# Optimization experiments

Hardware: AMD Instinct MI355X
Metric: run time of the kernel (lower is better)

The kernel has to match this reference:

```python
import jax, jax.numpy as jnp
import numpy as np

N, M, E, DIM = 100000, 2000, 400000, 128
GIN = 2 * DIM + 3  # gate MLP input width


def _mlp2(x, W1, b1, W2, b2):
    # Linear -> ReLU -> Linear
    return jnp.maximum(x @ W1 + b1, 0.0) @ W2 + b2


def setup_inputs() -> dict:
    key = jax.random.key(0)
    ks = jax.random.split(key, 20)
    s = lambda fan_in: 1.0 / np.sqrt(fan_in)
    inp = {
        "res_feat": jax.random.normal(ks[0], (N, DIM), jnp.float32),
        "meta_feat": jax.random.normal(ks[1], (M, DIM), jnp.float32),
        "sec_ids": jax.random.randint(ks[2], (N,), 0, M),
        "batch_pe_vector": jax.random.normal(ks[3], (N, 3), jnp.float32),
        "batch_meta_2_node_edge": jax.random.randint(ks[4], (2, E), 0, M),
        "batch_meta_2_node_vector": jax.random.normal(ks[5], (E, 3), jnp.float32),
        # gate1 params
        "g1_W1": jax.random.uniform(ks[6], (GIN, DIM), jnp.float32, -s(GIN), s(GIN)),
        "g1_b1": jnp.zeros((DIM,), jnp.float32),
        "g1_W2": jax.random.uniform(ks[7], (DIM, DIM), jnp.float32, -s(DIM), s(DIM)),
        "g1_b2": jnp.zeros((DIM,), jnp.float32),
        # gate2 params
        "g2_W1": jax.random.uniform(ks[8], (GIN, DIM), jnp.float32, -s(GIN), s(GIN)),
        "g2_b1": jnp.zeros((DIM,), jnp.float32),
        "g2_W2": jax.random.uniform(ks[9], (DIM, DIM), jnp.float32, -s(DIM), s(DIM)),
        "g2_b2": jnp.zeros((DIM,), jnp.float32),
        # fuse params
        "f_W1": jax.random.uniform(ks[10], (DIM, DIM), jnp.float32, -s(DIM), s(DIM)),
        "f_b1": jnp.zeros((DIM,), jnp.float32),
        "f_W2": jax.random.uniform(ks[11], (DIM, DIM), jnp.float32, -s(DIM), s(DIM)),
        "f_b2": jnp.zeros((DIM,), jnp.float32),
    }
    return inp


def reference(res_feat, meta_feat, sec_ids, batch_pe_vector,
              batch_meta_2_node_edge, batch_meta_2_node_vector,
              g1_W1, g1_b1, g1_W2, g1_b2,
              g2_W1, g2_b1, g2_W2, g2_b2,
              f_W1, f_b1, f_W2, f_b2):
    n = res_feat.shape[0]
    # gate1: per-node gather of meta features
    meta_broadcast = meta_feat[sec_ids]                       # [N, dim]
    gate1_in = jnp.concatenate([res_feat, meta_broadcast, -batch_pe_vector], axis=-1)
    gate1_w = _mlp2(gate1_in, g1_W1, g1_b1, g1_W2, g1_b2)     # [N, dim]
    # gate2: per-edge gathers
    src, dst = batch_meta_2_node_edge[0], batch_meta_2_node_edge[1]
    meta_add = meta_feat[src]                                 # [E, dim]
    res_b = res_feat[dst]                                     # [E, dim]
    gate2_in = jnp.concatenate([res_b, meta_add, batch_meta_2_node_vector], axis=-1)
    gate2_w = _mlp2(gate2_in, g2_W1, g2_b1, g2_W2, g2_b2)     # [E, dim]
    # scatter_mean over destination nodes
    vals = gate2_w * meta_add
    sums = jax.ops.segment_sum(vals, dst, num_segments=n)
    cnts = jax.ops.segment_sum(jnp.ones((vals.shape[0],), vals.dtype), dst, num_segments=n)
    meta_add_fea = sums / jnp.maximum(cnts, 1.0)[:, None]
    fused = res_feat + gate1_w * meta_broadcast + meta_add_fea
    return _mlp2(fused, f_W1, f_b1, f_W2, f_b2)
```

## Files before the change

### kernel.cpp

```cpp
#include <hip/hip_runtime.h>


typedef short bf16x8 __attribute__((ext_vector_type(8)));
typedef float f32x4  __attribute__((ext_vector_type(4)));

#define XS_PAD 136
#define F_PAD  132

__device__ __forceinline__ unsigned short f2bf(float f){
  union { float f; unsigned u; } v; v.f = f;
  return (unsigned short)((v.u + 0x7FFFu + ((v.u >> 16) & 1u)) >> 16);
}
__device__ __forceinline__ unsigned pack2(float a, float b){
  return (unsigned)f2bf(a) | ((unsigned)f2bf(b) << 16);
}
__device__ __forceinline__ float bf2f(unsigned short u){
  union { unsigned u; float f; } v; v.u = ((unsigned)u) << 16; return v.f;
}

__device__ __forceinline__ void mfma_layer(const unsigned short* Xs,
                                           const bf16x8 (&B)[2][4],
                                           int lane, f32x4 (&acc)[4][2]) {
  const int lcol = lane & 15, quad = lane >> 4;
  #pragma unroll
  for (int rg = 0; rg < 4; ++rg) {
    bf16x8 A[4];
    const unsigned short* ab = Xs + (rg*16 + lcol)*XS_PAD + quad*8;
    #pragma unroll
    for (int kk = 0; kk < 4; ++kk) A[kk] = *(const bf16x8*)(ab + kk*32);
    #pragma unroll
    for (int ctl = 0; ctl < 2; ++ctl)
      #pragma unroll
      for (int kk = 0; kk < 4; ++kk)
        acc[rg][ctl] = __builtin_amdgcn_mfma_f32_16x16x32_bf16(
            A[kk], B[ctl][kk], acc[rg][ctl], 0, 0, 0);
  }
}

__device__ __forceinline__ void load_bfrags(const unsigned short* __restrict__ Wt,
                                            int wave, int lane, bf16x8 (&B)[2][4]) {
  const int lcol = lane & 15, quad = lane >> 4;
  #pragma unroll
  for (int ctl = 0; ctl < 2; ++ctl) {
    int col = (wave*2 + ctl)*16 + lcol;
    #pragma unroll
    for (int kk = 0; kk < 4; ++kk)
      B[ctl][kk] = *(const bf16x8*)(Wt + (size_t)col*128 + kk*32 + quad*8);
  }
}

__device__ __forceinline__ void zero_acc(f32x4 (&acc)[4][2]) {
  #pragma unroll
  for (int rg = 0; rg < 4; ++rg)
    #pragma unroll
    for (int ctl = 0; ctl < 2; ++ctl) {
      acc[rg][ctl][0]=0.f; acc[rg][ctl][1]=0.f;
      acc[rg][ctl][2]=0.f; acc[rg][ctl][3]=0.f;
    }
}

struct WPtrs { const float* s[8]; };
__global__ __launch_bounds__(256) void transpose_w8(WPtrs p,
                                                    unsigned short* __restrict__ dstbase) {
  int slab = blockIdx.x >> 4, blk = blockIdx.x & 15;
  const float* W = p.s[slab];
  unsigned short* Wt = dstbase + (size_t)slab*16384;
  int c  = blk*8 + (threadIdx.x >> 5);
  int k0 = (threadIdx.x & 31) * 4;
  unsigned short o[4];
  #pragma unroll
  for (int j = 0; j < 4; ++j) o[j] = f2bf(W[(size_t)(k0 + j)*128 + c]);
  *(uint2*)(Wt + (size_t)c*128 + k0) =
      make_uint2((unsigned)o[0] | ((unsigned)o[1] << 16),
                 (unsigned)o[2] | ((unsigned)o[3] << 16));
}

__global__ __launch_bounds__(256) void a2_mfma(const float* __restrict__ res,
                                               const unsigned short* __restrict__ WAt,
                                               float* __restrict__ A2, int mrows) {
  __shared__ __align__(16) unsigned short Xs[64*XS_PAD];
  const int t = threadIdx.x, lane = t & 63, wave = t >> 6;
  const int quad = lane >> 4, lcol = lane & 15;
  const int tile0 = blockIdx.x * 64;
  bf16x8 B[2][4];
  load_bfrags(WAt, wave, lane, B);
  #pragma unroll
  for (int i = 0; i < 8; ++i) {
    int f = t + i*256, row = f >> 5, c4 = f & 31;
    int gr = tile0 + row;
    float4 v = make_float4(0.f,0.f,0.f,0.f);
    if (gr < mrows) v = *(const float4*)(res + (size_t)gr*128 + c4*4);
    *(uint2*)(Xs + row*XS_PAD + c4*4) = make_uint2(pack2(v.x,v.y), pack2(v.z,v.w));
  }
  __syncthreads();
  f32x4 acc[4][2]; zero_acc(acc);
  mfma_layer(Xs, B, lane, acc);
  #pragma unroll
  for (int rg = 0; rg < 4; ++rg)
    #pragma unroll
    for (int ctl = 0; ctl < 2; ++ctl) {
      int col = (wave*2 + ctl)*16 + lcol;
      #pragma unroll
      for (int reg = 0; reg < 4; ++reg) {
        int gr = tile0 + rg*16 + quad*4 + reg;
        if (gr < mrows) A2[(size_t)gr*128 + col] = acc[rg][ctl][reg];
      }
    }
}

__global__ void hist_kernel(const int* __restrict__ dst, int* __restrict__ counts, int E){
  int e = blockIdx.x*256 + threadIdx.x;
  if (e < E) atomicAdd(&counts[dst[e]], 1);
}
__global__ void scan1(const int* __restrict__ counts, int* __restrict__ exoff,
                      int* __restrict__ blocksum, int N){
  __shared__ int s[256];
  int t = threadIdx.x, gid = blockIdx.x*256 + t;
  int v = (gid < N) ? counts[gid] : 0;
  s[t] = v; __syncthreads();
  for (int off = 1; off < 256; off <<= 1){
    int x = (t >= off) ? s[t-off] : 0; __syncthreads();
    s[t] += x; __syncthreads();
  }
  if (gid < N) exoff[gid] = s[t] - v;
  if (t == 255) blocksum[blockIdx.x] = s[255];
}
__global__ void scan2(int* __restrict__ blocksum, int nb){
  __shared__ int s[512];
  int t = threadIdx.x;
  int v = (t < nb) ? blocksum[t] : 0;
  s[t] = v; __syncthreads();
  for (int off = 1; off < 512; off <<= 1){
    int x = (t >= off) ? s[t-off] : 0; __syncthreads();
    s[t] += x; __syncthreads();
  }
  if (t < nb) blocksum[t] = s[t] - v;
}
__global__ void scan3(int* __restrict__ exoff, const int* __restrict__ blockbase,
                      int* __restrict__ cursor, int N){
  int gid = blockIdx.x*256 + threadIdx.x;
  if (gid < N){ int v = exoff[gid] + blockbase[gid >> 8]; exoff[gid] = v; cursor[gid] = v; }
}
__global__ void fill_kernel(const int* __restrict__ dst, int* __restrict__ cursor,
                            int* __restrict__ edge_ids, int E){
  int e = blockIdx.x*256 + threadIdx.x;
  if (e < E){ int p = atomicAdd(&cursor[dst[e]], 1); edge_ids[p] = e; }
}

__global__ __launch_bounds__(256) void edge_mfma(
    const float* __restrict__ A2, const float* __restrict__ meta,
    const float* __restrict__ evec, const int* __restrict__ src,
    const int* __restrict__ edge_ids, const int* __restrict__ row_start,
    const int* __restrict__ counts,
    const float* __restrict__ g2W1full, const float* __restrict__ b1,
    const unsigned short* __restrict__ g2Bt, const unsigned short* __restrict__ W2t,
    const float* __restrict__ b2, float* __restrict__ SUM) {
  const int n = blockIdx.x;
  const int count = counts[n];
  if (count == 0) return;
  __shared__ __align__(16) unsigned short Xm[64*XS_PAD];
  __shared__ __align__(16) unsigned short Xh[64*XS_PAD];
  __shared__ __align__(16) float base[128];
  __shared__ __align__(16) float Wc[3*128];
  __shared__ float b2s[128];
  __shared__ int srcl[64];
  __shared__ float evl[64*3];
  const int t = threadIdx.x, lane = t & 63, wave = t >> 6;
  const int quad = lane >> 4, lcol = lane & 15;
  const int rs = row_start[n];

  bf16x8 BB[2][4], BW2[2][4];
  load_bfrags(g2Bt, wave, lane, BB);
  load_bfrags(W2t,  wave, lane, BW2);
  if (t < 128) {
    base[t]   = A2[(size_t)n*128 + t] + b1[t];
    b2s[t]    = b2[t];
    Wc[t]     = g2W1full[256*128 + t];
    Wc[128+t] = g2W1full[257*128 + t];
    Wc[256+t] = g2W1full[258*128 + t];
  }
  float sv0 = 0.f, sv1 = 0.f;

  for (int t0 = 0; t0 < count; t0 += 64) {
    __syncthreads();
    if (t < 64) {
      int idx = t0 + t;
      int s = 0; float e0=0.f,e1=0.f,e2=0.f;
      if (idx < count) {
        int e = edge_ids[rs + idx];
        s = src[e];
        e0 = evec[(size_t)e*3]; e1 = evec[(size_t)e*3+1]; e2 = evec[(size_t)e*3+2];
      }
      srcl[t] = s; evl[t*3] = e0; evl[t*3+1] = e1; evl[t*3+2] = e2;
    }
    __syncthreads();
    #pragma unroll
    for (int i = 0; i < 8; ++i) {
      int f = t + i*256, row = f >> 5, c4 = f & 31;
      float4 v = make_float4(0.f,0.f,0.f,0.f);
      if (t0 + row < count)
        v = *(const float4*)(meta + (size_t)srcl[row]*128 + c4*4);
      *(uint2*)(Xm + row*XS_PAD + c4*4) = make_uint2(pack2(v.x,v.y), pack2(v.z,v.w));
    }
    __syncthreads();
    f32x4 acc[4][2]; zero_acc(acc);
    mfma_layer(Xm, BB, lane, acc);
    #pragma unroll
    for (int rg = 0; rg < 4; ++rg)
      #pragma unroll
      for (int ctl = 0; ctl < 2; ++ctl) {
        int col = (wave*2 + ctl)*16 + lcol;
        #pragma unroll
        for (int reg = 0; reg < 4; ++reg) {
          int row = rg*16 + quad*4 + reg;
          float hv = acc[rg][ctl][reg] + base[col]
                   + evl[row*3]*Wc[col] + evl[row*3+1]*Wc[128+col]
                   + evl[row*3+2]*Wc[256+col];
          Xh[row*XS_PAD + col] = f2bf(fmaxf(hv, 0.f));
        }
      }
    __syncthreads();
    zero_acc(acc);
    mfma_layer(Xh, BW2, lane, acc);
    #pragma unroll
    for (int ctl = 0; ctl < 2; ++ctl) {
      int col = (wave*2 + ctl)*16 + lcol;
      float b2v = b2s[col];
      float s_acc = 0.f;
      #pragma unroll
      for (int rg = 0; rg < 4; ++rg)
        #pragma unroll
        for (int reg = 0; reg < 4; ++reg) {
          int rl = rg*16 + quad*4 + reg;
          if (t0 + rl < count)
            s_acc += (acc[rg][ctl][reg] + b2v) * bf2f(Xm[rl*XS_PAD + col]);
        }
      if (ctl == 0) sv0 += s_acc; else sv1 += s_acc;
    }
  }
  sv0 += __shfl_xor(sv0, 16, 64); sv0 += __shfl_xor(sv0, 32, 64);
  sv1 += __shfl_xor(sv1, 16, 64); sv1 += __shfl_xor(sv1, 32, 64);
  if (quad == 0) {
    SUM[(size_t)n*128 + (wave*2 + 0)*16 + lcol] = sv0;
    SUM[(size_t)n*128 + (wave*2 + 1)*16 + lcol] = sv1;
  }
}

__global__ __launch_bounds__(256) void fused_node(
    const float* __restrict__ res, const float* __restrict__ meta,
    const int* __restrict__ sec_ids, const float* __restrict__ pe,
    const float* __restrict__ g1W1full,
    const unsigned short* __restrict__ g1At, const unsigned short* __restrict__ g1Bt,
    const unsigned short* __restrict__ g1W2t, const float* __restrict__ g1b1,
    const float* __restrict__ g1b2,
    const unsigned short* __restrict__ fW1t, const float* __restrict__ fb1v,
    const unsigned short* __restrict__ fW2t, const float* __restrict__ fb2v,
    const float* __restrict__ SUM, const int* __restrict__ counts, int msize,
    float* __restrict__ out, int rows) {
  __shared__ __align__(16) unsigned short Xall[2*64*XS_PAD];
  unsigned short* Xa = Xall;
  unsigned short* Xm = Xall + 64*XS_PAD;
  float* F = (float*)Xall;
  __shared__ __align__(16) float Wc[3*128];
  __shared__ float b1s[128], b2s[128], fb1s[128], fb2s[128];
  __shared__ int   sids[64];
  __shared__ float pel[64*3];
  __shared__ float inv[64];
  const int t = threadIdx.x, lane = t & 63, wave = t >> 6;
  const int quad = lane >> 4, lcol = lane & 15;
  const int tile0 = blockIdx.x * 64;

  if (t < 128) {
    b1s[t] = g1b1[t]; b2s[t] = g1b2[t]; fb1s[t] = fb1v[t]; fb2s[t] = fb2v[t];
    Wc[t]     = g1W1full[256*128 + t];
    Wc[128+t] = g1W1full[257*128 + t];
    Wc[256+t] = g1W1full[258*128 + t];
  }
  if (t < 64) {
    int gr = tile0 + t;
    sids[t] = (gr < rows) ? sec_ids[gr] : 0;
    float p0=0.f,p1=0.f,p2=0.f;
    if (gr < rows){ p0=pe[(size_t)gr*3]; p1=pe[(size_t)gr*3+1]; p2=pe[(size_t)gr*3+2]; }
    pel[t*3]=p0; pel[t*3+1]=p1; pel[t*3+2]=p2;
    int c = (gr < rows && gr < msize) ? counts[gr] : 0;
    inv[t] = (c > 0) ? 1.f/(float)c : 0.f;
  }
  __syncthreads();

  bf16x8 BA[2][4], BB[2][4];
  load_bfrags(g1At, wave, lane, BA);
  load_bfrags(g1Bt, wave, lane, BB);

  #pragma unroll
  for (int i = 0; i < 8; ++i) {
    int f = t + i*256, row = f >> 5, c4 = f & 31;
    int gr = tile0 + row;
    float4 rv = make_float4(0.f,0.f,0.f,0.f);
    float4 mv = make_float4(0.f,0.f,0.f,0.f);
    if (gr < rows) {
      rv = *(const float4*)(res  + (size_t)gr*128 + c4*4);
      mv = *(const float4*)(meta + (size_t)sids[row]*128 + c4*4);
    }
    *(uint2*)(Xa + row*XS_PAD + c4*4) = make_uint2(pack2(rv.x,rv.y), pack2(rv.z,rv.w));
    *(uint2*)(Xm + row*XS_PAD + c4*4) = make_uint2(pack2(mv.x,mv.y), pack2(mv.z,mv.w));
  }
  __syncthreads();

  f32x4 acc[4][2]; zero_acc(acc);
  mfma_layer(Xa, BA, lane, acc);
  mfma_layer(Xm, BB, lane, acc);
  __syncthreads();
  #pragma unroll
  for (int rg = 0; rg < 4; ++rg)
    #pragma unroll
    for (int ctl = 0; ctl < 2; ++ctl) {
      int col = (wave*2 + ctl)*16 + lcol;
      #pragma unroll
      for (int reg = 0; reg < 4; ++reg) {
        int row = rg*16 + quad*4 + reg;
        float sm = b1s[col] - pel[row*3]*Wc[col]
                 - pel[row*3+1]*Wc[128+col] - pel[row*3+2]*Wc[256+col];
        Xa[row*XS_PAD + col] = f2bf(fmaxf(acc[rg][ctl][reg] + sm, 0.f));
      }
    }
  __syncthreads();
  bf16x8 B2g[2][4]; load_bfrags(g1W2t, wave, lane, B2g);
  zero_acc(acc);
  mfma_layer(Xa, B2g, lane, acc);
  __syncthreads();
  #pragma unroll
  for (int rg = 0; rg < 4; ++rg)
    #pragma unroll
    for (int ctl = 0; ctl < 2; ++ctl) {
      int col = (wave*2 + ctl)*16 + lcol;
      #pragma unroll
      for (int reg = 0; reg < 4; ++reg)
        Xa[(rg*16 + quad*4 + reg)*XS_PAD + col] = f2bf(acc[rg][ctl][reg] + b2s[col]);
    }
  __syncthreads();
  #pragma unroll
  for (int i = 0; i < 8; ++i) {
    int f = t + i*256, row = f >> 5, c4 = f & 31;
    int gr = tile0 + row;
    if (gr < rows) {
      float4 rv = *(const float4*)(res + (size_t)gr*128 + c4*4);
      uint2 gu = *(const uint2*)(Xa + row*XS_PAD + c4*4);
      uint2 mu = *(const uint2*)(Xm + row*XS_PAD + c4*4);
      float g0 = bf2f((unsigned short)(gu.x & 0xFFFF)), g1 = bf2f((unsigned short)(gu.x >> 16));
      float g2 = bf2f((unsigned short)(gu.y & 0xFFFF)), g3 = bf2f((unsigned short)(gu.y >> 16));
      float m0 = bf2f((unsigned short)(mu.x & 0xFFFF)), m1 = bf2f((unsigned short)(mu.x >> 16));
      float m2 = bf2f((unsigned short)(mu.y & 0xFFFF)), m3 = bf2f((unsigned short)(mu.y >> 16));
      float iv = inv[row];
      float s0=0.f,s1=0.f,s2=0.f,s3=0.f;
      if (iv > 0.f) {
        float4 s = *(const float4*)(SUM + (size_t)gr*128 + c4*4);
        s0 = s.x*iv; s1 = s.y*iv; s2 = s.z*iv; s3 = s.w*iv;
      }
      float f0 = rv.x + g0*m0 + s0, f1 = rv.y + g1*m1 + s1;
      float f2v = rv.z + g2*m2 + s2, f3 = rv.w + g3*m3 + s3;
      *(uint2*)(Xm + row*XS_PAD + c4*4) = make_uint2(pack2(f0,f1), pack2(f2v,f3));
    }
  }
  __syncthreads();
  bf16x8 BF1[2][4]; load_bfrags(fW1t, wave, lane, BF1);
  zero_acc(acc);
  mfma_layer(Xm, BF1, lane, acc);
  #pragma unroll
  for (int rg = 0; rg < 4; ++rg)
    #pragma unroll
    for (int ctl = 0; ctl < 2; ++ctl) {
      int col = (wave*2 + ctl)*16 + lcol;
      #pragma unroll
      for (int reg = 0; reg < 4; ++reg)
        Xa[(rg*16 + quad*4 + reg)*XS_PAD + col] =
            f2bf(fmaxf(acc[rg][ctl][reg] + fb1s[col], 0.f));
    }
  __syncthreads();
  bf16x8 BF2[2][4]; load_bfrags(fW2t, wave, lane, BF2);
  zero_acc(acc);
  mfma_layer(Xa, BF2, lane, acc);
  __syncthreads();
  #pragma unroll
  for (int rg = 0; rg < 4; ++rg)
    #pragma unroll
    for (int ctl = 0; ctl < 2; ++ctl) {
      int col = (wave*2 + ctl)*16 + lcol;
      #pragma unroll
      for (int reg = 0; reg < 4; ++reg)
        F[(rg*16 + quad*4 + reg)*F_PAD + col] = acc[rg][ctl][reg] + fb2s[col];
    }
  __syncthreads();
  #pragma unroll
  for (int i = 0; i < 8; ++i) {
    int f = t + i*256, row = f >> 5, c4 = f & 31;
    int gr = tile0 + row;
    if (gr < rows)
      *(float4*)(out + (size_t)gr*128 + c4*4) = *(const float4*)(F + row*F_PAD + c4*4);
  }
}

extern "C" void kernel_launch(void* const* d_in, const int* in_sizes, int n_in,
                              void* d_out, int out_size, void* d_ws, size_t ws_size,
                              hipStream_t stream) {
  const float* res     = (const float*)d_in[0];
  const float* meta    = (const float*)d_in[1];
  const int*   sec_ids = (const int*)  d_in[2];
  const float* pe      = (const float*)d_in[3];
  const int*   edge    = (const int*)  d_in[4];
  const float* evec    = (const float*)d_in[5];
  const float* g1W1 = (const float*)d_in[6];
  const float* g1b1 = (const float*)d_in[7];
  const float* g1W2 = (const float*)d_in[8];
  const float* g1b2 = (const float*)d_in[9];
  const float* g2W1 = (const float*)d_in[10];
  const float* g2b1 = (const float*)d_in[11];
  const float* g2W2 = (const float*)d_in[12];
  const float* g2b2 = (const float*)d_in[13];
  const float* fW1  = (const float*)d_in[14];
  const float* fb1  = (const float*)d_in[15];
  const float* fW2  = (const float*)d_in[16];
  const float* fb2  = (const float*)d_in[17];

  const int N = in_sizes[0] / 128;
  const int M = in_sizes[1] / 128;
  const int E = in_sizes[4] / 2;
  const int* src = edge;
  const int* dst = edge + E;

  float* ws = (float*)d_ws;
  float* A2   = ws;
  float* SUMb = A2 + (size_t)M*128;
  int* counts     = (int*)(SUMb + (size_t)M*128);
  int* row_startp = counts + M;
  int* cursor     = row_startp + M;
  int* blocksum   = cursor + M;
  int* edge_ids   = blocksum + 512;
  uintptr_t wp = (uintptr_t)(edge_ids + E);
  wp = (wp + 15) & ~(uintptr_t)15;
  unsigned short* Wt = (unsigned short*)wp;
  unsigned short* W_g1A  = Wt + 0*16384;
  unsigned short* W_g1B  = Wt + 1*16384;
  unsigned short* W_g1W2 = Wt + 2*16384;
  unsigned short* W_g2A  = Wt + 3*16384;
  unsigned short* W_g2B  = Wt + 4*16384;
  unsigned short* W_g2W2 = Wt + 5*16384;
  unsigned short* W_fW1  = Wt + 6*16384;
  unsigned short* W_fW2  = Wt + 7*16384;
  float* out = (float*)d_out;

  hipMemsetAsync(counts, 0, (size_t)M*sizeof(int), stream);
  hipMemsetAsync(SUMb, 0, (size_t)M*128*sizeof(float), stream);

  WPtrs p;
  p.s[0] = g1W1;            p.s[1] = g1W1 + 128*128;  p.s[2] = g1W2;
  p.s[3] = g2W1;            p.s[4] = g2W1 + 128*128;  p.s[5] = g2W2;
  p.s[6] = fW1;             p.s[7] = fW2;
  transpose_w8<<<128, 256, 0, stream>>>(p, Wt);

  const int nbMt = (M + 63) / 64;
  const int nbN  = (N + 63) / 64;
  const int nbE  = (E + 255) / 256;
  const int nbS  = (M + 255) / 256;

  a2_mfma<<<nbMt, 256, 0, stream>>>(res, W_g2A, A2, M);

  hist_kernel<<<nbE, 256, 0, stream>>>(dst, counts, E);
  scan1<<<nbS, 256, 0, stream>>>(counts, row_startp, blocksum, M);
  scan2<<<1, 512, 0, stream>>>(blocksum, nbS);
  scan3<<<nbS, 256, 0, stream>>>(row_startp, blocksum, cursor, M);
  fill_kernel<<<nbE, 256, 0, stream>>>(dst, cursor, edge_ids, E);

  edge_mfma<<<M, 256, 0, stream>>>(A2, meta, evec, src, edge_ids,
                                   row_startp, counts, g2W1, g2b1,
                                   W_g2B, W_g2W2, g2b2, SUMb);

  fused_node<<<nbN, 256, 0, stream>>>(res, meta, sec_ids, pe, g1W1,
                                      W_g1A, W_g1B, W_g1W2, g1b1, g1b2,
                                      W_fW1, fb1, W_fW2, fb2,
                                      SUMb, counts, M, out, N);
}
```

Before: 419.9 us.

## Precompute meta@W1B per meta row, split edge segments across blocks with atomics

New measurement: 400.6 us. 4.6% less time.

```diff
diff --git a/kernel.cpp b/kernel.cpp
--- a/kernel.cpp
+++ b/kernel.cpp
@@ -5,7 +5,7 @@
 typedef float f32x4  __attribute__((ext_vector_type(4)));
 
 #define XS_PAD 136
-#define F_PAD  132
+#define S_SPLIT 4
 
 __device__ __forceinline__ unsigned short f2bf(float f){
   union { float f; unsigned u; } v; v.f = f;
@@ -75,21 +75,27 @@
                  (unsigned)o[2] | ((unsigned)o[3] << 16));
 }
 
-__global__ __launch_bounds__(256) void a2_mfma(const float* __restrict__ res,
-                                               const unsigned short* __restrict__ WAt,
-                                               float* __restrict__ A2, int mrows) {
+__global__ __launch_bounds__(256) void prep_mfma(const float* __restrict__ res,
+                                                 const float* __restrict__ meta,
+                                                 const unsigned short* __restrict__ WAt,
+                                                 const unsigned short* __restrict__ WBt,
+                                                 float* __restrict__ A2,
+                                                 float* __restrict__ M2, int mrows) {
   __shared__ __align__(16) unsigned short Xs[64*XS_PAD];
   const int t = threadIdx.x, lane = t & 63, wave = t >> 6;
   const int quad = lane >> 4, lcol = lane & 15;
   const int tile0 = blockIdx.x * 64;
+  const float* X = blockIdx.y ? meta : res;
+  const unsigned short* Wt = blockIdx.y ? WBt : WAt;
+  float* Y = blockIdx.y ? M2 : A2;
   bf16x8 B[2][4];
-  load_bfrags(WAt, wave, lane, B);
+  load_bfrags(Wt, wave, lane, B);
   #pragma unroll
   for (int i = 0; i < 8; ++i) {
     int f = t + i*256, row = f >> 5, c4 = f & 31;
     int gr = tile0 + row;
     float4 v = make_float4(0.f,0.f,0.f,0.f);
-    if (gr < mrows) v = *(const float4*)(res + (size_t)gr*128 + c4*4);
+    if (gr < mrows) v = *(const float4*)(X + (size_t)gr*128 + c4*4);
     *(uint2*)(Xs + row*XS_PAD + c4*4) = make_uint2(pack2(v.x,v.y), pack2(v.z,v.w));
   }
   __syncthreads();
@@ -103,7 +109,7 @@
       #pragma unroll
       for (int reg = 0; reg < 4; ++reg) {
         int gr = tile0 + rg*16 + quad*4 + reg;
-        if (gr < mrows) A2[(size_t)gr*128 + col] = acc[rg][ctl][reg];
+        if (gr < mrows) Y[(size_t)gr*128 + col] = acc[rg][ctl][reg];
       }
     }
 }
@@ -148,45 +154,47 @@
 }
 
 __global__ __launch_bounds__(256) void edge_mfma(
-    const float* __restrict__ A2, const float* __restrict__ meta,
-    const float* __restrict__ evec, const int* __restrict__ src,
-    const int* __restrict__ edge_ids, const int* __restrict__ row_start,
-    const int* __restrict__ counts,
-    const float* __restrict__ g2W1full, const float* __restrict__ b1,
-    const unsigned short* __restrict__ g2Bt, const unsigned short* __restrict__ W2t,
-    const float* __restrict__ b2, float* __restrict__ SUM) {
-  const int n = blockIdx.x;
+    const float* __restrict__ A2, const float* __restrict__ M2,
+    const float* __restrict__ meta, const float* __restrict__ evec,
+    const int* __restrict__ src, const int* __restrict__ edge_ids,
+    const int* __restrict__ row_start, const int* __restrict__ counts,
+    const float* __restrict__ b1, const float* __restrict__ g2W1full,
+    const unsigned short* __restrict__ W2t, const float* __restrict__ b2,
+    float* __restrict__ SUM) {
+  const int n = blockIdx.x / S_SPLIT, k = blockIdx.x % S_SPLIT;
   const int count = counts[n];
-  if (count == 0) return;
-  __shared__ __align__(16) unsigned short Xm[64*XS_PAD];
+  const int per = (count + S_SPLIT - 1) / S_SPLIT;
+  const int lo = k * per;
+  int hi = lo + per; if (hi > count) hi = count;
+  const int cnt = hi - lo;
+  if (cnt <= 0) return;
+  const int rs = row_start[n] + lo;
+
   __shared__ __align__(16) unsigned short Xh[64*XS_PAD];
-  __shared__ __align__(16) float base[128];
-  __shared__ __align__(16) float Wc[3*128];
-  __shared__ float b2s[128];
   __shared__ int srcl[64];
   __shared__ float evl[64*3];
   const int t = threadIdx.x, lane = t & 63, wave = t >> 6;
   const int quad = lane >> 4, lcol = lane & 15;
-  const int rs = row_start[n];
-
-  bf16x8 BB[2][4], BW2[2][4];
-  load_bfrags(g2Bt, wave, lane, BB);
-  load_bfrags(W2t,  wave, lane, BW2);
-  if (t < 128) {
-    base[t]   = A2[(size_t)n*128 + t] + b1[t];
-    b2s[t]    = b2[t];
-    Wc[t]     = g2W1full[256*128 + t];
-    Wc[128+t] = g2W1full[257*128 + t];
-    Wc[256+t] = g2W1full[258*128 + t];
-  }
-  float sv0 = 0.f, sv1 = 0.f;
-
-  for (int t0 = 0; t0 < count; t0 += 64) {
+  const int c0 = (t & 31) * 4, rbase = t >> 5;
+
+  bf16x8 BW2[2][4];
+  load_bfrags(W2t, wave, lane, BW2);
+  float4 a2v = *(const float4*)(A2 + (size_t)n*128 + c0);
+  float4 b1v = *(const float4*)(b1 + c0);
+  float4 base = make_float4(a2v.x+b1v.x, a2v.y+b1v.y, a2v.z+b1v.z, a2v.w+b1v.w);
+  float4 w0 = *(const float4*)(g2W1full + 256*128 + c0);
+  float4 w1 = *(const float4*)(g2W1full + 257*128 + c0);
+  float4 w2 = *(const float4*)(g2W1full + 258*128 + c0);
+  const int colA = wave*32 + lcol, colB = colA + 16;
+  const float b2A = b2[colA], b2B = b2[colB];
+  float psA = 0.f, psB = 0.f;
+
+  for (int t0 = 0; t0 < cnt; t0 += 64) {
     __syncthreads();
     if (t < 64) {
       int idx = t0 + t;
       int s = 0; float e0=0.f,e1=0.f,e2=0.f;
-      if (idx < count) {
+      if (idx < cnt) {
         int e = edge_ids[rs + idx];
         s = src[e];
         e0 = evec[(size_t)e*3]; e1 = evec[(size_t)e*3+1]; e2 = evec[(size_t)e*3+2];
@@ -196,53 +204,39 @@
     __syncthreads();
     #pragma unroll
     for (int i = 0; i < 8; ++i) {
-      int f = t + i*256, row = f >> 5, c4 = f & 31;
-      float4 v = make_float4(0.f,0.f,0.f,0.f);
-      if (t0 + row < count)
-        v = *(const float4*)(meta + (size_t)srcl[row]*128 + c4*4);
-      *(uint2*)(Xm + row*XS_PAD + c4*4) = make_uint2(pack2(v.x,v.y), pack2(v.z,v.w));
+      int row = rbase + 8*i;
+      float4 h = make_float4(0.f,0.f,0.f,0.f);
+      if (t0 + row < cnt) {
+        int s = srcl[row];
+        float4 m = *(const float4*)(M2 + (size_t)s*128 + c0);
+        float e0 = evl[row*3], e1 = evl[row*3+1], e2 = evl[row*3+2];
+        h.x = fmaxf(base.x + m.x + e0*w0.x + e1*w1.x + e2*w2.x, 0.f);
+        h.y = fmaxf(base.y + m.y + e0*w0.y + e1*w1.y + e2*w2.y, 0.f);
+        h.z = fmaxf(base.z + m.z + e0*w0.z + e1*w1.z + e2*w2.z, 0.f);
+        h.w = fmaxf(base.w + m.w + e0*w0.w + e1*w1.w + e2*w2.w, 0.f);
+      }
+      *(uint2*)(Xh + row*XS_PAD + c0) = make_uint2(pack2(h.x,h.y), pack2(h.z,h.w));
     }
     __syncthreads();
     f32x4 acc[4][2]; zero_acc(acc);
-    mfma_layer(Xm, BB, lane, acc);
+    mfma_layer(Xh, BW2, lane, acc);
     #pragma unroll
     for (int rg = 0; rg < 4; ++rg)
       #pragma unroll
-      for (int ctl = 0; ctl < 2; ++ctl) {
-        int col = (wave*2 + ctl)*16 + lcol;
-        #pragma unroll
-        for (int reg = 0; reg < 4; ++reg) {
-          int row = rg*16 + quad*4 + reg;
-          float hv = acc[rg][ctl][reg] + base[col]
-                   + evl[row*3]*Wc[col] + evl[row*3+1]*Wc[128+col]
-                   + evl[row*3+2]*Wc[256+col];
-          Xh[row*XS_PAD + col] = f2bf(fmaxf(hv, 0.f));
+      for (int reg = 0; reg < 4; ++reg) {
+        int rl = rg*16 + quad*4 + reg;
+        if (t0 + rl < cnt) {
+          int s = srcl[rl];
+          psA += (acc[rg][0][reg] + b2A) * meta[(size_t)s*128 + colA];
+          psB += (acc[rg][1][reg] + b2B) * meta[(size_t)s*128 + colB];
         }
       }
-    __syncthreads();
-    zero_acc(acc);
-    mfma_layer(Xh, BW2, lane, acc);
-    #pragma unroll
-    for (int ctl = 0; ctl < 2; ++ctl) {
-      int col = (wave*2 + ctl)*16 + lcol;
-      float b2v = b2s[col];
-      float s_acc = 0.f;
-      #pragma unroll
-      for (int rg = 0; rg < 4; ++rg)
-        #pragma unroll
-        for (int reg = 0; reg < 4; ++reg) {
-          int rl = rg*16 + quad*4 + reg;
-          if (t0 + rl < count)
-            s_acc += (acc[rg][ctl][reg] + b2v) * bf2f(Xm[rl*XS_PAD + col]);
-        }
-      if (ctl == 0) sv0 += s_acc; else sv1 += s_acc;
-    }
-  }
-  sv0 += __shfl_xor(sv0, 16, 64); sv0 += __shfl_xor(sv0, 32, 64);
-  sv1 += __shfl_xor(sv1, 16, 64); sv1 += __shfl_xor(sv1, 32, 64);
+  }
+  psA += __shfl_xor(psA, 16, 64); psA += __shfl_xor(psA, 32, 64);
+  psB += __shfl_xor(psB, 16, 64); psB += __shfl_xor(psB, 32, 64);
   if (quad == 0) {
-    SUM[(size_t)n*128 + (wave*2 + 0)*16 + lcol] = sv0;
-    SUM[(size_t)n*128 + (wave*2 + 1)*16 + lcol] = sv1;
+    atomicAdd(&SUM[(size_t)n*128 + colA], psA);
+    atomicAdd(&SUM[(size_t)n*128 + colB], psB);
   }
 }
 
@@ -257,25 +251,16 @@
     const unsigned short* __restrict__ fW2t, const float* __restrict__ fb2v,
     const float* __restrict__ SUM, const int* __restrict__ counts, int msize,
     float* __restrict__ out, int rows) {
-  __shared__ __align__(16) unsigned short Xall[2*64*XS_PAD];
-  unsigned short* Xa = Xall;
-  unsigned short* Xm = Xall + 64*XS_PAD;
-  float* F = (float*)Xall;
-  __shared__ __align__(16) float Wc[3*128];
-  __shared__ float b1s[128], b2s[128], fb1s[128], fb2s[128];
+  __shared__ __align__(16) unsigned short Xa[64*XS_PAD];
+  __shared__ __align__(16) unsigned short Xm[64*XS_PAD];
   __shared__ int   sids[64];
   __shared__ float pel[64*3];
   __shared__ float inv[64];
   const int t = threadIdx.x, lane = t & 63, wave = t >> 6;
   const int quad = lane >> 4, lcol = lane & 15;
   const int tile0 = blockIdx.x * 64;
-
-  if (t < 128) {
-    b1s[t] = g1b1[t]; b2s[t] = g1b2[t]; fb1s[t] = fb1v[t]; fb2s[t] = fb2v[t];
-    Wc[t]     = g1W1full[256*128 + t];
-    Wc[128+t] = g1W1full[257*128 + t];
-    Wc[256+t] = g1W1full[258*128 + t];
-  }
+  const int c0 = (t & 31) * 4, rbase = t >> 5;
+
   if (t < 64) {
     int gr = tile0 + t;
     sids[t] = (gr < rows) ? sec_ids[gr] : 0;
@@ -285,24 +270,32 @@
     int c = (gr < rows && gr < msize) ? counts[gr] : 0;
     inv[t] = (c > 0) ? 1.f/(float)c : 0.f;
   }
-  __syncthreads();
-
+  const int colA = wave*32 + lcol, colB = colA + 16;
+  const float b1A = g1b1[colA],  b1B = g1b1[colB];
+  const float b2A = g1b2[colA],  b2B = g1b2[colB];
+  const float fb1A = fb1v[colA], fb1B = fb1v[colB];
+  const float fb2A = fb2v[colA], fb2B = fb2v[colB];
+  const float wA0 = g1W1full[256*128+colA], wA1 = g1W1full[257*128+colA],
+              wA2 = g1W1full[258*128+colA];
+  const float wB0 = g1W1full[256*128+colB], wB1 = g1W1full[257*128+colB],
+              wB2 = g1W1full[258*128+colB];
   bf16x8 BA[2][4], BB[2][4];
   load_bfrags(g1At, wave, lane, BA);
   load_bfrags(g1Bt, wave, lane, BB);
+  __syncthreads();
 
   #pragma unroll
   for (int i = 0; i < 8; ++i) {
-    int f = t + i*256, row = f >> 5, c4 = f & 31;
+    int row = rbase + 8*i;
     int gr = tile0 + row;
     float4 rv = make_float4(0.f,0.f,0.f,0.f);
     float4 mv = make_float4(0.f,0.f,0.f,0.f);
     if (gr < rows) {
-      rv = *(const float4*)(res  + (size_t)gr*128 + c4*4);
-      mv = *(const float4*)(meta + (size_t)sids[row]*128 + c4*4);
-    }
-    *(uint2*)(Xa + row*XS_PAD + c4*4) = make_uint2(pack2(rv.x,rv.y), pack2(rv.z,rv.w));
-    *(uint2*)(Xm + row*XS_PAD + c4*4) = make_uint2(pack2(mv.x,mv.y), pack2(mv.z,mv.w));
+      rv = *(const float4*)(res  + (size_t)gr*128 + c0);
+      mv = *(const float4*)(meta + (size_t)sids[row]*128 + c0);
+    }
+    *(uint2*)(Xa + row*XS_PAD + c0) = make_uint2(pack2(rv.x,rv.y), pack2(rv.z,rv.w));
+    *(uint2*)(Xm + row*XS_PAD + c0) = make_uint2(pack2(mv.x,mv.y), pack2(mv.z,mv.w));
   }
   __syncthreads();
 
@@ -313,15 +306,13 @@
   #pragma unroll
   for (int rg = 0; rg < 4; ++rg)
     #pragma unroll
-    for (int ctl = 0; ctl < 2; ++ctl) {
-      int col = (wave*2 + ctl)*16 + lcol;
-      #pragma unroll
-      for (int reg = 0; reg < 4; ++reg) {
-        int row = rg*16 + quad*4 + reg;
-        float sm = b1s[col] - pel[row*3]*Wc[col]
-                 - pel[row*3+1]*Wc[128+col] - pel[row*3+2]*Wc[256+col];
-        Xa[row*XS_PAD + col] = f2bf(fmaxf(acc[rg][ctl][reg] + sm, 0.f));
-      }
+    for (int reg = 0; reg < 4; ++reg) {
+      int row = rg*16 + quad*4 + reg;
+      float p0 = pel[row*3], p1 = pel[row*3+1], p2 = pel[row*3+2];
+      float vA = acc[rg][0][reg] + b1A - p0*wA0 - p1*wA1 - p2*wA2;
+      float vB = acc[rg][1][reg] + b1B - p0*wB0 - p1*wB1 - p2*wB2;
+      Xa[row*XS_PAD + colA] = f2bf(fmaxf(vA, 0.f));
+      Xa[row*XS_PAD + colB] = f2bf(fmaxf(vB, 0.f));
     }
   __syncthreads();
   bf16x8 B2g[2][4]; load_bfrags(g1W2t, wave, lane, B2g);
@@ -331,21 +322,20 @@
   #pragma unroll
   for (int rg = 0; rg < 4; ++rg)
     #pragma unroll
-    for (int ctl = 0; ctl < 2; ++ctl) {
-      int col = (wave*2 + ctl)*16 + lcol;
-      #pragma unroll
-      for (int reg = 0; reg < 4; ++reg)
-        Xa[(rg*16 + quad*4 + reg)*XS_PAD + col] = f2bf(acc[rg][ctl][reg] + b2s[col]);
+    for (int reg = 0; reg < 4; ++reg) {
+      int row = rg*16 + quad*4 + reg;
+      Xa[row*XS_PAD + colA] = f2bf(acc[rg][0][reg] + b2A);
+      Xa[row*XS_PAD + colB] = f2bf(acc[rg][1][reg] + b2B);
     }
   __syncthreads();
   #pragma unroll
   for (int i = 0; i < 8; ++i) {
-    int f = t + i*256, row = f >> 5, c4 = f & 31;
+    int row = rbase + 8*i;
     int gr = tile0 + row;
     if (gr < rows) {
-      float4 rv = *(const float4*)(res + (size_t)gr*128 + c4*4);
-      uint2 gu = *(const uint2*)(Xa + row*XS_PAD + c4*4);
-      uint2 mu = *(const uint2*)(Xm + row*XS_PAD + c4*4);
+      float4 rv = *(const float4*)(res + (size_t)gr*128 + c0);
+      uint2 gu = *(const uint2*)(Xa + row*XS_PAD + c0);
+      uint2 mu = *(const uint2*)(Xm + row*XS_PAD + c0);
       float g0 = bf2f((unsigned short)(gu.x & 0xFFFF)), g1 = bf2f((unsigned short)(gu.x >> 16));
       float g2 = bf2f((unsigned short)(gu.y & 0xFFFF)), g3 = bf2f((unsigned short)(gu.y >> 16));
       float m0 = bf2f((unsigned short)(mu.x & 0xFFFF)), m1 = bf2f((unsigned short)(mu.x >> 16));
@@ -353,12 +343,12 @@
       float iv = inv[row];
       float s0=0.f,s1=0.f,s2=0.f,s3=0.f;
       if (iv > 0.f) {
-        float4 s = *(const float4*)(SUM + (size_t)gr*128 + c4*4);
+        float4 s = *(const float4*)(SUM + (size_t)gr*128 + c0);
         s0 = s.x*iv; s1 = s.y*iv; s2 = s.z*iv; s3 = s.w*iv;
       }
       float f0 = rv.x + g0*m0 + s0, f1 = rv.y + g1*m1 + s1;
       float f2v = rv.z + g2*m2 + s2, f3 = rv.w + g3*m3 + s3;
-      *(uint2*)(Xm + row*XS_PAD + c4*4) = make_uint2(pack2(f0,f1), pack2(f2v,f3));
+      *(uint2*)(Xm + row*XS_PAD + c0) = make_uint2(pack2(f0,f1), pack2(f2v,f3));
     }
   }
   __syncthreads();
@@ -368,35 +358,25 @@
   #pragma unroll
   for (int rg = 0; rg < 4; ++rg)
     #pragma unroll
-    for (int ctl = 0; ctl < 2; ++ctl) {
-      int col = (wave*2 + ctl)*16 + lcol;
-      #pragma unroll
-      for (int reg = 0; reg < 4; ++reg)
-        Xa[(rg*16 + quad*4 + reg)*XS_PAD + col] =
-            f2bf(fmaxf(acc[rg][ctl][reg] + fb1s[col], 0.f));
+    for (int reg = 0; reg < 4; ++reg) {
+      int row = rg*16 + quad*4 + reg;
+      Xa[row*XS_PAD + colA] = f2bf(fmaxf(acc[rg][0][reg] + fb1A, 0.f));
+      Xa[row*XS_PAD + colB] = f2bf(fmaxf(acc[rg][1][reg] + fb1B, 0.f));
     }
   __syncthreads();
   bf16x8 BF2[2][4]; load_bfrags(fW2t, wave, lane, BF2);
   zero_acc(acc);
   mfma_layer(Xa, BF2, lane, acc);
-  __syncthreads();
-  #pragma unroll
-  for (int rg = 0; rg < 4; ++rg)
-    #pragma unroll
-    for (int ctl = 0; ctl < 2; ++ctl) {
-      int col = (wave*2 + ctl)*16 + lcol;
-      #pragma unroll
-      for (int reg = 0; reg < 4; ++reg)
-        F[(rg*16 + quad*4 + reg)*F_PAD + col] = acc[rg][ctl][reg] + fb2s[col];
-    }
-  __syncthreads();
-  #pragma unroll
-  for (int i = 0; i < 8; ++i) {
-    int f = t + i*256, row = f >> 5, c4 = f & 31;
-    int gr = tile0 + row;
-    if (gr < rows)
-      *(float4*)(out + (size_t)gr*128 + c4*4) = *(const float4*)(F + row*F_PAD + c4*4);
-  }
+  #pragma unroll
+  for (int rg = 0; rg < 4; ++rg)
+    #pragma unroll
+    for (int reg = 0; reg < 4; ++reg) {
+      int gr = tile0 + rg*16 + quad*4 + reg;
+      if (gr < rows) {
+        out[(size_t)gr*128 + colA] = acc[rg][0][reg] + fb2A;
+        out[(size_t)gr*128 + colB] = acc[rg][1][reg] + fb2B;
+      }
+    }
 }
 
 extern "C" void kernel_launch(void* const* d_in, const int* in_sizes, int n_in,
@@ -429,7 +409,8 @@
 
   float* ws = (float*)d_ws;
   float* A2   = ws;
-  float* SUMb = A2 + (size_t)M*128;
+  float* M2   = A2 + (size_t)M*128;
+  float* SUMb = M2 + (size_t)M*128;
   int* counts     = (int*)(SUMb + (size_t)M*128);
   int* row_startp = counts + M;
   int* cursor     = row_startp + M;
@@ -462,7 +443,7 @@
   const int nbE  = (E + 255) / 256;
   const int nbS  = (M + 255) / 256;
 
-  a2_mfma<<<nbMt, 256, 0, stream>>>(res, W_g2A, A2, M);
+  prep_mfma<<<dim3(nbMt, 2), 256, 0, stream>>>(res, meta, W_g2A, W_g2B, A2, M2, M);
 
   hist_kernel<<<nbE, 256, 0, stream>>>(dst, counts, E);
   scan1<<<nbS, 256, 0, stream>>>(counts, row_startp, blocksum, M);
@@ -470,9 +451,9 @@
   scan3<<<nbS, 256, 0, stream>>>(row_startp, blocksum, cursor, M);
   fill_kernel<<<nbE, 256, 0, stream>>>(dst, cursor, edge_ids, E);
 
-  edge_mfma<<<M, 256, 0, stream>>>(A2, meta, evec, src, edge_ids,
-                                   row_startp, counts, g2W1, g2b1,
-                                   W_g2B, W_g2W2, g2b2, SUMb);
+  edge_mfma<<<M*S_SPLIT, 256, 0, stream>>>(A2, M2, meta, evec, src, edge_ids,
+                                           row_startp, counts, g2b1, g2W1,
+                                           W_g2W2, g2b2, SUMb);
 
   fused_node<<<nbN, 256, 0, stream>>>(res, meta, sec_ids, pe, g1W1,
                                       W_g1A, W_g1B, W_g1W2, g1b1, g1b2,
```
